# Kernel optimization log

Hardware: AMD Instinct MI355X
Metric: run time of the kernel (lower is better)

The kernel has to match this reference:

```python
import jax, jax.numpy as jnp
import numpy as np
from jax import lax

L, T, DM, DH = 4, 4096, 2048, 1024
MAX_PHASE = 6.28
EPS = 1e-5


def setup_inputs() -> dict:
    key = jax.random.key(0)
    ks = jax.random.split(key, 16)
    # LRU initializers (r_min=0, r_max=1)
    u1 = jax.random.uniform(ks[0], (L, DH))
    nu_log = jnp.log(-0.5 * jnp.log(u1))
    u2 = jax.random.uniform(ks[1], (L, DH))
    theta_log = jnp.log(MAX_PHASE * u2)
    abs_lam = jnp.exp(-jnp.exp(nu_log))  # |lambda|
    gamma_log = jnp.log(jnp.sqrt(1.0 - abs_lam ** 2))
    B_re = jax.random.normal(ks[2], (L, DH, DM)) / np.sqrt(2 * DM)
    B_im = jax.random.normal(ks[3], (L, DH, DM)) / np.sqrt(2 * DM)
    C_re = jax.random.normal(ks[4], (L, DM, DH)) / np.sqrt(DH)
    C_im = jax.random.normal(ks[5], (L, DM, DH)) / np.sqrt(DH)
    D = jax.random.normal(ks[6], (L, DM))
    bound = 1.0 / np.sqrt(DM)
    enc_w = jax.random.uniform(ks[7], (DM, DM), minval=-bound, maxval=bound)
    enc_b = jax.random.uniform(ks[8], (DM,), minval=-bound, maxval=bound)
    out1_w = jax.random.uniform(ks[9], (L, DM, DM), minval=-bound, maxval=bound)
    out1_b = jax.random.uniform(ks[10], (L, DM), minval=-bound, maxval=bound)
    out2_w = jax.random.uniform(ks[11], (L, DM, DM), minval=-bound, maxval=bound)
    out2_b = jax.random.uniform(ks[12], (L, DM), minval=-bound, maxval=bound)
    norm_w = jnp.ones((L, DM))
    norm_b = jnp.zeros((L, DM))
    x = jax.random.normal(ks[13], (T, DM))
    return dict(x=x, enc_w=enc_w, enc_b=enc_b, nu_log=nu_log, theta_log=theta_log,
                gamma_log=gamma_log, B_re=B_re, B_im=B_im, C_re=C_re, C_im=C_im,
                D=D, norm_w=norm_w, norm_b=norm_b, out1_w=out1_w, out1_b=out1_b,
                out2_w=out2_w, out2_b=out2_b)


def _lru(xn, nu, th, gl, br, bi, cr, ci, d):
    # xn: (T, DM) real -> (T, DM) real
    lam = jnp.exp(-jnp.exp(nu) + 1j * jnp.exp(th))          # (DH,) complex
    B_norm = (br + 1j * bi) * jnp.exp(gl)[:, None]           # (DH, DM)
    Bu = xn.astype(B_norm.dtype) @ B_norm.T                  # (T, DH) complex
    a = jnp.broadcast_to(lam, Bu.shape)
    def combine(e1, e2):
        a1, b1 = e1
        a2, b2 = e2
        return a1 * a2, a2 * b1 + b2
    _, h = lax.associative_scan(combine, (a, Bu), axis=0)    # h_t = lam*h_{t-1} + Bu_t
    C = cr + 1j * ci
    return (h @ C.T).real + xn * d


def _batchnorm(x, w, b):
    # training-mode BatchNorm1d over dim 0 (biased variance), matching torch
    mu = x.mean(axis=0)
    var = jnp.mean((x - mu) ** 2, axis=0)
    return (x - mu) / jnp.sqrt(var + EPS) * w + b


def _forward(x, enc_w, enc_b, nu_log, theta_log, gamma_log, B_re, B_im,
             C_re, C_im, D, norm_w, norm_b, out1_w, out1_b, out2_w, out2_b):
    x = x @ enc_w.T + enc_b
    def layer(carry, p):
        nu, th, gl, br, bi, cr, ci, d, nw, nb, w1, b1, w2, b2 = p
        xn = _batchnorm(carry, nw, nb)
        y = _lru(xn, nu, th, gl, br, bi, cr, ci, d)
        y = jax.nn.gelu(y, approximate=False)
        y = (y @ w1.T + b1) * jax.nn.sigmoid(y @ w2.T + b2)
        return carry + y, None
    x, _ = lax.scan(layer, x, (nu_log, theta_log, gamma_log, B_re, B_im,
                               C_re, C_im, D, norm_w, norm_b,
                               out1_w, out1_b, out2_w, out2_b))
    return x


def reference(x, enc_w, enc_b, nu_log, theta_log, gamma_log, B_re, B_im,
              C_re, C_im, D, norm_w, norm_b, out1_w, out1_b, out2_w, out2_b):
    return _forward(x, enc_w, enc_b, nu_log, theta_log, gamma_log, B_re, B_im,
                    C_re, C_im, D, norm_w, norm_b, out1_w, out1_b, out2_w, out2_b)
```

## Files before the change

kernel.cpp:

```cpp
#include <hip/hip_runtime.h>
#include <stdint.h>
#include <math.h>


#define LAYERS 4
#define TT     4096
#define DMODEL 2048
#define DHID   1024
#define NCHUNK 64
#define CLEN   64
#define KTILES 64

typedef unsigned short ushort_t;
typedef __attribute__((ext_vector_type(8))) _Float16 half8;
typedef __attribute__((ext_vector_type(4))) float    f32x4;

__device__ __forceinline__ unsigned pack2h(float a, float b) {
  _Float16 ha = (_Float16)a, hb = (_Float16)b;
  unsigned short ua = *(unsigned short*)&ha, ub = *(unsigned short*)&hb;
  return (unsigned)ua | ((unsigned)ub << 16);
}

__global__ __launch_bounds__(256)
void convert_h(const float* __restrict__ B0, const float* __restrict__ B1,
               int ldb, int NS, int KS, ushort_t* __restrict__ Hi)
{
  __shared__ float tile[128][33];
  const int mb  = blockIdx.x;
  const int kb  = blockIdx.y;
  const int tid = threadIdx.x;
  const int r0  = tid >> 3;
  const int c0  = (tid & 7) * 4;
#pragma unroll
  for (int rep = 0; rep < 4; ++rep) {
    const int rr = rep * 32 + r0;
    const int n  = mb * 128 + rr;
    const int k  = kb * 32 + c0;
    const float* bp; long idx;
    if (n >= NS)      { bp = B1; idx = (long)(n - NS) * ldb + k; }
    else if (k >= KS) { bp = B1; idx = (long)n * ldb + (k - KS); }
    else              { bp = B0; idx = (long)n * ldb + k; }
#pragma unroll
    for (int u = 0; u < 4; ++u) tile[rr][c0 + u] = bp[idx + u];
  }
  __syncthreads();
#pragma unroll
  for (int rep = 0; rep < 2; ++rep) {
    const int id2 = rep * 256 + tid;
    const int kg  = id2 >> 7;
    const int m   = id2 & 127;
    const long off = ((long)mb * KTILES + kb) * 4096 + (kg * 128 + m) * 8;
    unsigned hw[4];
#pragma unroll
    for (int p = 0; p < 4; ++p)
      hw[p] = pack2h(tile[m][kg * 8 + p * 2], tile[m][kg * 8 + p * 2 + 1]);
    *(uint4*)&Hi[off] = make_uint4(hw[0], hw[1], hw[2], hw[3]);
  }
}

__global__ __launch_bounds__(256)
void bn_convert(const float* __restrict__ carry, const float* __restrict__ stats,
                const float* __restrict__ nw, const float* __restrict__ nb,
                float* __restrict__ act, ushort_t* __restrict__ Hi)
{
  __shared__ float tile[128][33];
  const int mb  = blockIdx.x;
  const int kb  = blockIdx.y;
  const int tid = threadIdx.x;
  const int r0  = tid >> 3;
  const int c0  = (tid & 7) * 4;
  float mean[4], rstd[4], w_[4], b_[4];
#pragma unroll
  for (int u = 0; u < 4; ++u) {
    const int j = kb * 32 + c0 + u;
    const float mu = stats[j] * (1.0f / TT);
    const float va = fmaxf(stats[DMODEL + j] * (1.0f / TT) - mu * mu, 0.0f);
    mean[u] = mu; rstd[u] = rsqrtf(va + 1e-5f);
    w_[u] = nw[j]; b_[u] = nb[j];
  }
#pragma unroll
  for (int rep = 0; rep < 4; ++rep) {
    const int rr  = rep * 32 + r0;
    const long base = (long)(mb * 128 + rr) * 2048 + kb * 32 + c0;
#pragma unroll
    for (int u = 0; u < 4; ++u) {
      const float v = (carry[base + u] - mean[u]) * rstd[u] * w_[u] + b_[u];
      tile[rr][c0 + u] = v;
      act[base + u] = v;
    }
  }
  __syncthreads();
#pragma unroll
  for (int rep = 0; rep < 2; ++rep) {
    const int id2 = rep * 256 + tid;
    const int kg  = id2 >> 7;
    const int m   = id2 & 127;
    const long off = ((long)mb * KTILES + kb) * 4096 + (kg * 128 + m) * 8;
    unsigned hw[4];
#pragma unroll
    for (int p = 0; p < 4; ++p)
      hw[p] = pack2h(tile[m][kg * 8 + p * 2], tile[m][kg * 8 + p * 2 + 1]);
    *(uint4*)&Hi[off] = make_uint4(hw[0], hw[1], hw[2], hw[3]);
  }
}

__global__ __launch_bounds__(256)
void e1_convert(const float* __restrict__ y, const float* __restrict__ xn,
                const float* __restrict__ d, ushort_t* __restrict__ Hi)
{
  __shared__ float tile[128][33];
  const int mb  = blockIdx.x;
  const int kb  = blockIdx.y;
  const int tid = threadIdx.x;
  const int r0  = tid >> 3;
  const int c0  = (tid & 7) * 4;
  float dv[4];
#pragma unroll
  for (int u = 0; u < 4; ++u) dv[u] = d[kb * 32 + c0 + u];
#pragma unroll
  for (int rep = 0; rep < 4; ++rep) {
    const int rr  = rep * 32 + r0;
    const long base = (long)(mb * 128 + rr) * 2048 + kb * 32 + c0;
#pragma unroll
    for (int u = 0; u < 4; ++u) {
      const float v = y[base + u] + xn[base + u] * dv[u];
      tile[rr][c0 + u] = 0.5f * v * (1.0f + erff(v * 0.70710678118654752440f));
    }
  }
  __syncthreads();
#pragma unroll
  for (int rep = 0; rep < 2; ++rep) {
    const int id2 = rep * 256 + tid;
    const int kg  = id2 >> 7;
    const int m   = id2 & 127;
    const long off = ((long)mb * KTILES + kb) * 4096 + (kg * 128 + m) * 8;
    unsigned hw[4];
#pragma unroll
    for (int p = 0; p < 4; ++p)
      hw[p] = pack2h(tile[m][kg * 8 + p * 2], tile[m][kg * 8 + p * 2 + 1]);
    *(uint4*)&Hi[off] = make_uint4(hw[0], hw[1], hw[2], hw[3]);
  }
}

#define GLDS(gp, lp) __builtin_amdgcn_global_load_lds( \
    (__attribute__((address_space(1))) void*)(void*)(gp), \
    (__attribute__((address_space(3))) void*)(lp), 16, 0, 0)

__global__ __launch_bounds__(256)
void gemm_mfma(const ushort_t* __restrict__ Ahi, const ushort_t* __restrict__ Bhi,
               float* __restrict__ C, const float* __restrict__ bias,
               int epi, const float* __restrict__ aux)
{
  __shared__ ushort_t S[2][16384];
  const int tid  = threadIdx.x;
  const int lane = tid & 63;
  const int wid  = tid >> 6;
  const int wm   = wid >> 1;
  const int wn   = wid & 1;

  const int bid = blockIdx.y * gridDim.x + blockIdx.x;
  const int xcd = bid & 7, idx = bid >> 3;
  const int mb  = ((xcd & 3) << 3) | (idx & 7);
  const int nb  = ((xcd >> 2) << 3) | (idx >> 3);

  f32x4 acc[4][4];
#pragma unroll
  for (int i = 0; i < 4; ++i)
#pragma unroll
    for (int j = 0; j < 4; ++j) acc[i][j] = (f32x4){0.f, 0.f, 0.f, 0.f};

  const ushort_t* ga = Ahi + (long)mb * KTILES * 4096 + tid * 8;
  const ushort_t* gb = Bhi + (long)nb * KTILES * 4096 + tid * 8;

  const int albase = ((lane >> 4) * 128 + wm * 64 + (lane & 15)) * 8;
  const int blbase = ((lane >> 4) * 128 + wn * 64 + (lane & 15)) * 8;

  half8 A0[4], B0[4], A1[4], B1[4];

#define STAGE(P) \
  GLDS(ga,        &S[P][tid * 8]); \
  GLDS(ga + 2048, &S[P][2048 + tid * 8]); \
  GLDS(ga + 4096, &S[P][4096 + tid * 8]); \
  GLDS(ga + 6144, &S[P][6144 + tid * 8]); \
  GLDS(gb,        &S[P][8192 + tid * 8]); \
  GLDS(gb + 2048, &S[P][10240 + tid * 8]); \
  GLDS(gb + 4096, &S[P][12288 + tid * 8]); \
  GLDS(gb + 6144, &S[P][14336 + tid * 8]); \
  ga += 8192; gb += 8192;

#define RD(P) \
  _Pragma("unroll") \
  for (int m = 0; m < 4; ++m) A0[m] = *(const half8*)&S[P][albase + m * 128]; \
  _Pragma("unroll") \
  for (int n = 0; n < 4; ++n) B0[n] = *(const half8*)&S[P][8192 + blbase + n * 128]; \
  _Pragma("unroll") \
  for (int m = 0; m < 4; ++m) A1[m] = *(const half8*)&S[P][4096 + albase + m * 128]; \
  _Pragma("unroll") \
  for (int n = 0; n < 4; ++n) B1[n] = *(const half8*)&S[P][12288 + blbase + n * 128];

#define MFMA16(A_, B_) \
  _Pragma("unroll") \
  for (int m = 0; m < 4; ++m) \
    _Pragma("unroll") \
    for (int n = 0; n < 4; ++n) \
      acc[m][n] = __builtin_amdgcn_mfma_f32_16x16x32_f16(A_[m], B_[n], acc[m][n], 0, 0, 0);

#define WAIT_VM_BAR(n) asm volatile("s_waitcnt vmcnt(" #n ")" ::: "memory"); \
  __builtin_amdgcn_sched_barrier(0); __builtin_amdgcn_s_barrier();
#define LGKM0_BAR asm volatile("s_waitcnt lgkmcnt(0)" ::: "memory"); \
  __builtin_amdgcn_sched_barrier(0); __builtin_amdgcn_s_barrier();

#define KSTEP(P) \
  WAIT_VM_BAR(8) \
  RD(P) \
  __builtin_amdgcn_s_setprio(1); \
  MFMA16(A0, B0) \
  MFMA16(A1, B1) \
  __builtin_amdgcn_s_setprio(0); \
  LGKM0_BAR \
  STAGE(P)

  STAGE(0)
  STAGE(1)

  for (int it = 0; it < 15; ++it) {
    KSTEP(0)
    KSTEP(1)
  }
  WAIT_VM_BAR(8)
  RD(0)
  __builtin_amdgcn_s_setprio(1);
  MFMA16(A0, B0)
  MFMA16(A1, B1)
  __builtin_amdgcn_s_setprio(0);
  WAIT_VM_BAR(0)
  RD(1)
  __builtin_amdgcn_s_setprio(1);
  MFMA16(A0, B0)
  MFMA16(A1, B1)
  __builtin_amdgcn_s_setprio(0);
#undef STAGE
#undef RD
#undef MFMA16
#undef WAIT_VM_BAR
#undef LGKM0_BAR
#undef KSTEP

  const int cn = lane & 15;
  const int cr = (lane >> 4) * 4;
#pragma unroll
  for (int m = 0; m < 4; ++m) {
    const long row = (long)mb * 128 + wm * 64 + m * 16 + cr;
#pragma unroll
    for (int n = 0; n < 4; ++n) {
      const int col = nb * 128 + wn * 64 + n * 16 + cn;
      const float bv = bias ? bias[col] : 0.0f;
      if (epi == 0) {
#pragma unroll
        for (int q = 0; q < 4; ++q)
          C[(row + q) * 2048 + col] = acc[m][n][q] + bv;
      } else if (epi == 1) {
#pragma unroll
        for (int q = 0; q < 4; ++q)
          C[(row + q) * 2048 + col] = 1.0f / (1.0f + expf(-(acc[m][n][q] + bv)));
      } else {
#pragma unroll
        for (int q = 0; q < 4; ++q) {
          const long idx2 = (row + q) * 2048 + col;
          C[idx2] += (acc[m][n][q] + bv) * aux[idx2];
        }
      }
    }
  }
}

__global__ void bn_partial(const float* __restrict__ carry, float* __restrict__ stats)
{
  const int j  = blockIdx.x * 256 + threadIdx.x;
  const int r0 = blockIdx.y * 128;
  float s = 0.f, ss = 0.f;
  for (int r = 0; r < 128; ++r) {
    float v = carry[(long)(r0 + r) * DMODEL + j];
    s += v; ss += v * v;
  }
  atomicAdd(&stats[j], s);
  atomicAdd(&stats[DMODEL + j], ss);
}

__device__ __forceinline__ void get_lam(const float* nu_log, const float* th_log,
                                        int h, float& lre, float& lim)
{
  const float mag = expf(-expf(nu_log[h]));
  const float th  = expf(th_log[h]);
  lre = mag * cosf(th);
  lim = mag * sinf(th);
}

__global__ void scan1(float* __restrict__ bu,
                      const float* __restrict__ nu_log, const float* __restrict__ th_log,
                      const float* __restrict__ gl_log)
{
  const int gid = blockIdx.x * 256 + threadIdx.x;
  const int c = gid >> 10, h = gid & 1023;
  float lre, lim; get_lam(nu_log, th_log, h, lre, lim);
  const float gamma = expf(gl_log[h]);
  float hr = 0.f, hi = 0.f;
  for (int i = 0; i < CLEN; ++i) {
    const long t = (long)c * CLEN + i;
    const float br_ = bu[t * 2048 + h] * gamma;
    const float bi_ = bu[t * 2048 + 1024 + h] * gamma;
    const float nr = lre * hr - lim * hi + br_;
    const float ni = lre * hi + lim * hr + bi_;
    hr = nr; hi = ni;
    bu[t * 2048 + h] = hr;
    bu[t * 2048 + 1024 + h] = hi;
  }
}

__global__ void scan2(const float* __restrict__ loc,
                      float* __restrict__ ccre, float* __restrict__ ccim,
                      const float* __restrict__ nu_log, const float* __restrict__ th_log)
{
  const int h = blockIdx.x * 256 + threadIdx.x;
  float lre, lim; get_lam(nu_log, th_log, h, lre, lim);
  float ar = lre, ai = lim;
  for (int s = 0; s < 6; ++s) { float nr = ar * ar - ai * ai, ni = 2.f * ar * ai; ar = nr; ai = ni; }
  float er = 0.f, ei = 0.f;
  for (int c = 0; c < NCHUNK; ++c) {
    ccre[c * DHID + h] = er; ccim[c * DHID + h] = ei;
    const long t = (long)c * CLEN + (CLEN - 1);
    const float nr = ar * er - ai * ei + loc[t * 2048 + h];
    const float ni = ar * ei + ai * er + loc[t * 2048 + 1024 + h];
    er = nr; ei = ni;
  }
}

__global__ void scan3(float* __restrict__ loc,
                      const float* __restrict__ ccre, const float* __restrict__ ccim,
                      const float* __restrict__ nu_log, const float* __restrict__ th_log)
{
  const int gid = blockIdx.x * 256 + threadIdx.x;
  const int c = gid >> 10, h = gid & 1023;
  float lre, lim; get_lam(nu_log, th_log, h, lre, lim);
  const float cr_ = ccre[c * DHID + h], ci_ = ccim[c * DHID + h];
  float pr = lre, pi = lim;
  for (int i = 0; i < CLEN; ++i) {
    const long t = (long)c * CLEN + i;
    const float hre = loc[t * 2048 + h]        + pr * cr_ - pi * ci_;
    const float him = loc[t * 2048 + 1024 + h] + pr * ci_ + pi * cr_;
    const float npr = pr * lre - pi * lim, npi = pr * lim + pi * lre;
    pr = npr; pi = npi;
    loc[t * 2048 + h]        = hre;
    loc[t * 2048 + 1024 + h] = -him;
  }
}

__global__ void finalize(const float* __restrict__ carry, float* __restrict__ out)
{
  const long idx = (long)blockIdx.x * 256 + threadIdx.x;
  const float v = carry[idx];
  out[idx] = (v == v && fabsf(v) < 3.0e38f) ? v : 300000.0f;
}

__global__ void diagfill(float* __restrict__ out, float val)
{
  const long idx = (long)blockIdx.x * 256 + threadIdx.x;
  out[idx] = (idx == 0) ? val : 0.0f;
}

extern "C" void kernel_launch(void* const* d_in, const int* in_sizes, int n_in,
                              void* d_out, int out_size, void* d_ws, size_t ws_size,
                              hipStream_t stream)
{
  (void)out_size;
  const int EW = (TT * DMODEL) / 256;
  float* out = (float*)d_out;

  if (n_in != 17 || in_sizes[0] != TT * DMODEL) {
    diagfill<<<EW, 256, 0, stream>>>(out, (float)(1 << 18));
    return;
  }
  if (ws_size < 151600000ull) {
    diagfill<<<EW, 256, 0, stream>>>(out, (float)(1 << 12));
    return;
  }

  const float* x     = (const float*)d_in[0];
  const float* enc_w = (const float*)d_in[1];
  const float* enc_b = (const float*)d_in[2];
  const float* nu    = (const float*)d_in[3];
  const float* th    = (const float*)d_in[4];
  const float* gl    = (const float*)d_in[5];
  const float* Bre   = (const float*)d_in[6];
  const float* Bim   = (const float*)d_in[7];
  const float* Cre   = (const float*)d_in[8];
  const float* Cim   = (const float*)d_in[9];
  const float* Dd    = (const float*)d_in[10];
  const float* nw    = (const float*)d_in[11];
  const float* nb    = (const float*)d_in[12];
  const float* w1    = (const float*)d_in[13];
  const float* b1    = (const float*)d_in[14];
  const float* w2    = (const float*)d_in[15];
  const float* b2    = (const float*)d_in[16];

  char* ws = (char*)d_ws;
  float*    carry = (float*)(ws);
  float*    act   = (float*)(ws + 33554432);
  float*    buf1  = (float*)(ws + 67108864);
  ushort_t* Ahi   = (ushort_t*)(ws + 100663296);
  ushort_t* Bhi   = (ushort_t*)(ws + 134217728);
  float*    ccre  = (float*)(ws + 150994944);
  float*    ccim  = (float*)(ws + 151257088);
  float*    stats = (float*)(ws + 151519232);

  const dim3 gcA(32, 64);
  const dim3 gcW(16, 64);
  const dim3 gg(32, 16);
  const int BIG = 1 << 30;

  convert_h<<<gcA, 256, 0, stream>>>(x, x, 2048, BIG, BIG, Ahi);
  convert_h<<<gcW, 256, 0, stream>>>(enc_w, enc_w, 2048, BIG, BIG, Bhi);
  gemm_mfma<<<gg, 256, 0, stream>>>(Ahi, Bhi, carry, enc_b, 0, nullptr);

  for (int l = 0; l < LAYERS; ++l) {
    const float* Brl = Bre + (size_t)l * DHID * DMODEL;
    const float* Bil = Bim + (size_t)l * DHID * DMODEL;
    const float* Crl = Cre + (size_t)l * DMODEL * DHID;
    const float* Cil = Cim + (size_t)l * DMODEL * DHID;
    const float* w1l = w1 + (size_t)l * DMODEL * DMODEL;
    const float* w2l = w2 + (size_t)l * DMODEL * DMODEL;

    hipMemsetAsync(stats, 0, 2 * DMODEL * sizeof(float), stream);
    bn_partial<<<dim3(DMODEL / 256, TT / 128), 256, 0, stream>>>(carry, stats);
    bn_convert<<<gcA, 256, 0, stream>>>(carry, stats, nw + l * DMODEL, nb + l * DMODEL,
                                        act, Ahi);

    convert_h<<<gcW, 256, 0, stream>>>(Brl, Bil, 2048, 1024, BIG, Bhi);
    gemm_mfma<<<gg, 256, 0, stream>>>(Ahi, Bhi, buf1, nullptr, 0, nullptr);

    scan1<<<256, 256, 0, stream>>>(buf1, nu + l * DHID, th + l * DHID, gl + l * DHID);
    scan2<<<4, 256, 0, stream>>>(buf1, ccre, ccim, nu + l * DHID, th + l * DHID);
    scan3<<<256, 256, 0, stream>>>(buf1, ccre, ccim, nu + l * DHID, th + l * DHID);

    convert_h<<<gcA, 256, 0, stream>>>(buf1, buf1, 2048, BIG, BIG, Ahi);
    convert_h<<<gcW, 256, 0, stream>>>(Crl, Cil, 1024, BIG, 1024, Bhi);
    gemm_mfma<<<gg, 256, 0, stream>>>(Ahi, Bhi, buf1, nullptr, 0, nullptr);

    e1_convert<<<gcA, 256, 0, stream>>>(buf1, act, Dd + l * DMODEL, Ahi);

    convert_h<<<gcW, 256, 0, stream>>>(w2l, w2l, 2048, BIG, BIG, Bhi);
    gemm_mfma<<<gg, 256, 0, stream>>>(Ahi, Bhi, act, b2 + l * DMODEL, 1, nullptr);

    convert_h<<<gcW, 256, 0, stream>>>(w1l, w1l, 2048, BIG, BIG, Bhi);
    gemm_mfma<<<gg, 256, 0, stream>>>(Ahi, Bhi, carry, b1 + l * DMODEL, 2, act);
  }

  finalize<<<EW, 256, 0, stream>>>(carry, out);
}
```

Measured before the change: 1.441 ms.

## Fuse gated output GEMMs into one dual-B kernel sharing A tiles

Replaces the two separate out1/out2 GEMMs (sigmoid gate written to act, then multiply-accumulate into carry) with a single kernel that loads each A tile once and computes both products. The gate is applied in registers and the result is added to carry in the epilogue. This removes the fp32 write and reread of the gate tensor and one pass over A. It uses a 3-stage LDS pipeline with two accumulator sets, which doubles accumulator registers and may lower occupancy.

```diff
diff --git a/kernel.cpp b/kernel.cpp
--- a/kernel.cpp
+++ b/kernel.cpp
@@ -222,7 +222,6 @@
 
   STAGE(0)
   STAGE(1)
-
   for (int it = 0; it < 15; ++it) {
     KSTEP(0)
     KSTEP(1)
@@ -274,6 +273,124 @@
   }
 }
 
+__global__ __launch_bounds__(256)
+void gemm_dual(const ushort_t* __restrict__ Ahi, const ushort_t* __restrict__ B1t,
+               const ushort_t* __restrict__ B2t,
+               float* __restrict__ carry, const float* __restrict__ b1,
+               const float* __restrict__ b2)
+{
+  __shared__ ushort_t S[3][12288];
+  const int tid  = threadIdx.x;
+  const int lane = tid & 63;
+  const int wid  = tid >> 6;
+  const int wm   = wid >> 1;
+  const int wn   = wid & 1;
+
+  const int bid = blockIdx.y * gridDim.x + blockIdx.x;
+  const int xcd = bid & 7, idx = bid >> 3;
+  const int mb  = ((xcd & 3) << 3) | (idx & 7);
+  const int nb  = ((xcd >> 2) << 3) | (idx >> 3);
+
+  f32x4 acc1[4][4], acc2[4][4];
+#pragma unroll
+  for (int i = 0; i < 4; ++i)
+#pragma unroll
+    for (int j = 0; j < 4; ++j) {
+      acc1[i][j] = (f32x4){0.f, 0.f, 0.f, 0.f};
+      acc2[i][j] = (f32x4){0.f, 0.f, 0.f, 0.f};
+    }
+
+  const ushort_t* ga = Ahi + (long)mb * KTILES * 4096 + tid * 8;
+  const ushort_t* g1 = B1t + (long)nb * KTILES * 4096 + tid * 8;
+  const ushort_t* g2 = B2t + (long)nb * KTILES * 4096 + tid * 8;
+
+  const int albase = ((lane >> 4) * 128 + wm * 64 + (lane & 15)) * 8;
+  const int blbase = ((lane >> 4) * 128 + wn * 64 + (lane & 15)) * 8;
+
+  half8 Af[4], B1f[4], B2f[4];
+
+#define STAGE(P) \
+  GLDS(ga,        &S[P][tid * 8]); \
+  GLDS(ga + 2048, &S[P][2048 + tid * 8]); \
+  GLDS(g1,        &S[P][4096 + tid * 8]); \
+  GLDS(g1 + 2048, &S[P][6144 + tid * 8]); \
+  GLDS(g2,        &S[P][8192 + tid * 8]); \
+  GLDS(g2 + 2048, &S[P][10240 + tid * 8]); \
+  ga += 4096; g1 += 4096; g2 += 4096;
+
+#define RD(P) \
+  _Pragma("unroll") \
+  for (int m = 0; m < 4; ++m) Af[m]  = *(const half8*)&S[P][albase + m * 128]; \
+  _Pragma("unroll") \
+  for (int n = 0; n < 4; ++n) B1f[n] = *(const half8*)&S[P][4096 + blbase + n * 128]; \
+  _Pragma("unroll") \
+  for (int n = 0; n < 4; ++n) B2f[n] = *(const half8*)&S[P][8192 + blbase + n * 128];
+
+#define MFMA32D \
+  __builtin_amdgcn_s_setprio(1); \
+  _Pragma("unroll") \
+  for (int m = 0; m < 4; ++m) \
+    _Pragma("unroll") \
+    for (int n = 0; n < 4; ++n) \
+      acc1[m][n] = __builtin_amdgcn_mfma_f32_16x16x32_f16(Af[m], B1f[n], acc1[m][n], 0, 0, 0); \
+  _Pragma("unroll") \
+  for (int m = 0; m < 4; ++m) \
+    _Pragma("unroll") \
+    for (int n = 0; n < 4; ++n) \
+      acc2[m][n] = __builtin_amdgcn_mfma_f32_16x16x32_f16(Af[m], B2f[n], acc2[m][n], 0, 0, 0); \
+  __builtin_amdgcn_s_setprio(0);
+
+#define WAITB(n) asm volatile("s_waitcnt vmcnt(" #n ") lgkmcnt(0)" ::: "memory"); \
+  __builtin_amdgcn_sched_barrier(0); __builtin_amdgcn_s_barrier();
+
+#define KSTEPD(PRD, PST) \
+  WAITB(6) \
+  STAGE(PST) \
+  RD(PRD) \
+  MFMA32D
+
+  STAGE(0)
+  STAGE(1)
+
+  for (int it = 0; it < 20; ++it) {
+    KSTEPD(0, 2)
+    KSTEPD(1, 0)
+    KSTEPD(2, 1)
+  }
+  KSTEPD(0, 2)
+  KSTEPD(1, 0)
+  WAITB(6)
+  RD(2)
+  MFMA32D
+  WAITB(0)
+  RD(0)
+  MFMA32D
+#undef STAGE
+#undef RD
+#undef MFMA32D
+#undef WAITB
+#undef KSTEPD
+
+  const int cn = lane & 15;
+  const int cr = (lane >> 4) * 4;
+#pragma unroll
+  for (int m = 0; m < 4; ++m) {
+    const long row = (long)mb * 128 + wm * 64 + m * 16 + cr;
+#pragma unroll
+    for (int n = 0; n < 4; ++n) {
+      const int col = nb * 128 + wn * 64 + n * 16 + cn;
+      const float b1v = b1[col], b2v = b2[col];
+#pragma unroll
+      for (int q = 0; q < 4; ++q) {
+        const long idx2 = (row + q) * 2048 + col;
+        const float t1v = acc1[m][n][q] + b1v;
+        const float t2v = acc2[m][n][q] + b2v;
+        carry[idx2] += t1v * (1.0f / (1.0f + expf(-t2v)));
+      }
+    }
+  }
+}
+
 __global__ void bn_partial(const float* __restrict__ carry, float* __restrict__ stats)
 {
   const int j  = blockIdx.x * 256 + threadIdx.x;
@@ -408,6 +525,7 @@
   float*    act   = (float*)(ws + 33554432);
   float*    buf1  = (float*)(ws + 67108864);
   ushort_t* Ahi   = (ushort_t*)(ws + 100663296);
+  ushort_t* B2hi  = (ushort_t*)(ws + 117440512);
   ushort_t* Bhi   = (ushort_t*)(ws + 134217728);
   float*    ccre  = (float*)(ws + 150994944);
   float*    ccim  = (float*)(ws + 151257088);
@@ -448,11 +566,10 @@
 
     e1_convert<<<gcA, 256, 0, stream>>>(buf1, act, Dd + l * DMODEL, Ahi);
 
-    convert_h<<<gcW, 256, 0, stream>>>(w2l, w2l, 2048, BIG, BIG, Bhi);
-    gemm_mfma<<<gg, 256, 0, stream>>>(Ahi, Bhi, act, b2 + l * DMODEL, 1, nullptr);
-
     convert_h<<<gcW, 256, 0, stream>>>(w1l, w1l, 2048, BIG, BIG, Bhi);
-    gemm_mfma<<<gg, 256, 0, stream>>>(Ahi, Bhi, carry, b1 + l * DMODEL, 2, act);
+    convert_h<<<gcW, 256, 0, stream>>>(w2l, w2l, 2048, BIG, BIG, B2hi);
+    gemm_dual<<<gg, 256, 0, stream>>>(Ahi, Bhi, B2hi, carry,
+                                      b1 + l * DMODEL, b2 + l * DMODEL);
   }
 
   finalize<<<EW, 256, 0, stream>>>(carry, out);
```

New measurement: 1.422 ms. About the same (-1.4%).
